# Kernel tuning notes

Measured on AMD Instinct MI355X. Metric: run time of the kernel, lower is better.

## Reference

```python
import jax, jax.numpy as jnp
import numpy as np

NUM_HEADS = 16
HEAD_DIM = 32  # out_ch 512 / 16 heads

def _c(x):
    # last axis holds (real, imag) -> complex64
    return jax.lax.complex(x[..., 0], x[..., 1])

def setup_inputs() -> dict:
    key = jax.random.key(0)
    ks = jax.random.split(key, 9)
    B, S, C = 1, 2048, 512
    mk = lambda k, shp: jax.random.normal(k, shp, dtype=jnp.float32)
    return {
        "Q": mk(ks[0], (B, S, C, 2)),
        "V": mk(ks[1], (B, S, C, 2)),
        "K": mk(ks[2], (B, S, C, 2)),
        "Wq": mk(ks[3], (C, C, 2)) * (1.0 / np.sqrt(C)),
        "bq": mk(ks[4], (C, 2)) * 0.02,
        "Wk": mk(ks[5], (C, C, 2)) * (1.0 / np.sqrt(C)),
        "bk": mk(ks[6], (C, 2)) * 0.02,
        "Wv": mk(ks[7], (C, C, 2)) * (1.0 / np.sqrt(C)),
        "bv": mk(ks[8], (C, 2)) * 0.02,
    }

def _split_heads(x):
    B, S, D = x.shape
    return x.reshape(B, S, NUM_HEADS, HEAD_DIM).transpose(0, 2, 1, 3)  # [B,H,S,d]

def reference(Q, V, K, Wq, bq, Wk, bk, Wv, bv):
    Qc, Kc, Vc = _c(Q), _c(K), _c(V)
    # torch Linear: y = x @ W^T + b, W is [out, in]
    proj = lambda x, W, b: jnp.einsum('bsi,oi->bso', x, _c(W)) + _c(b)
    q = _split_heads(proj(Qc, Wq, bq))  # [B,H,S,d] complex64
    k = _split_heads(proj(Kc, Wk, bk))
    v = _split_heads(proj(Vc, Wv, bv))
    scores = jnp.einsum('bhqd,bhkd->bhqk', q, jnp.conj(k)) / np.sqrt(HEAD_DIM).astype(np.float32)
    weights = jax.nn.softmax(jnp.abs(scores), axis=-1)  # real [B,H,S,S]
    out = jnp.einsum('bhqk,bhkd->bhqd', weights.astype(v.dtype), v)  # complex
    B, H, S, d = out.shape
    out = out.transpose(0, 2, 1, 3).reshape(B, S, H * d)  # [B,S,out_ch]
    return jnp.stack([out.real, out.imag], axis=-1)  # [B,S,out_ch,2] float32
```

## Files before the change

kernel.cpp:

```cpp
#include <hip/hip_runtime.h>
#include <hip/hip_bf16.h>
#include <math.h>

#define S_LEN 2048
#define C_DIM 512
#define NH 16
#define HD 32
#define PLANE_U (NH * S_LEN * HD)
#define WPL 262144

typedef __attribute__((ext_vector_type(8)))  short bf16x8;
typedef __attribute__((ext_vector_type(4)))  float f32x4;
typedef __attribute__((ext_vector_type(16))) float f32x16;
typedef __attribute__((ext_vector_type(4)))  unsigned int u32x4;

#if __has_builtin(__builtin_amdgcn_exp2f)
#define EXP2(x) __builtin_amdgcn_exp2f(x)
#else
#define EXP2(x) exp2f(x)
#endif

__device__ __forceinline__ unsigned int pk_bf16(float a, float b) {
    float2 f; f.x = a; f.y = b;
    __hip_bfloat162 t = __float22bfloat162_rn(f);
    return *reinterpret_cast<unsigned int*>(&t);
}

__global__ __launch_bounds__(256)
void wcvt(const float* __restrict__ Wq, const float* __restrict__ Wk,
          const float* __restrict__ Wv, unsigned short* __restrict__ ws)
{
    const int tid = blockIdx.x*256 + threadIdx.x;
    const int z   = tid >> 15;
    const int rem = tid & 32767;
    const int row = rem >> 6;
    const int kc  = (rem & 63) * 8;
    const float2* w2 = (const float2*)(z == 0 ? Wq : (z == 1 ? Wk : Wv));
    const float4* s4 = (const float4*)(w2 + (size_t)row*C_DIM + kc);
    float4 f0 = s4[0], f1 = s4[1], f2v = s4[2], f3 = s4[3];
    float re[8] = {f0.x,f0.z,f1.x,f1.z,f2v.x,f2v.z,f3.x,f3.z};
    float im[8] = {f0.y,f0.w,f1.y,f1.w,f2v.y,f2v.w,f3.y,f3.w};
    u32x4 rh, ih;
    #pragma unroll
    for (int p2 = 0; p2 < 4; ++p2) {
        rh[p2] = pk_bf16(re[2*p2], re[2*p2+1]);
        ih[p2] = pk_bf16(im[2*p2], im[2*p2+1]);
    }
    unsigned short* wf = ws + 6*(size_t)PLANE_U;
    const size_t off = (size_t)row*C_DIM + kc;
    *(u32x4*)&wf[(size_t)(z*2+0)*WPL + off] = rh;
    *(u32x4*)&wf[(size_t)(z*2+1)*WPL + off] = ih;
}

#define PROW2 72

__global__ __launch_bounds__(256)
void proj_mfma(const float* __restrict__ Q, const float* __restrict__ V,
               const float* __restrict__ K,
               const float* __restrict__ bq, const float* __restrict__ bk,
               const float* __restrict__ bv,
               unsigned short* __restrict__ ws)
{
    const int z = blockIdx.z;
    const float *X, *b;
    if (z == 0)      { X = Q; b = bq; }
    else if (z == 1) { X = K; b = bk; }
    else             { X = V; b = bv; }

    const int s0 = blockIdx.x * 64;
    const int o0 = blockIdx.y * 64;

    const float2* Bsrc = (const float2*)X;
    const unsigned short* wf = ws + 6*(size_t)PLANE_U;
    const size_t pb = (size_t)z*2*WPL;

    __shared__ __align__(16) unsigned short LBrh[64*PROW2], LBih[64*PROW2];

    const int t    = threadIdx.x;
    const int wave = t >> 6;
    const int lr   = t & 15;
    const int g    = (t & 63) >> 4;
    const int srow = t >> 2;
    const int skc  = (t & 3) * 16;

    const f32x4 zf = {0.f,0.f,0.f,0.f};
    f32x4 accR[4], accI[4];
    #pragma unroll
    for (int i = 0; i < 4; ++i) { accR[i] = zf; accI[i] = zf; }

    const size_t arow = (size_t)(o0 + wave*16 + lr) * C_DIM;

    for (int k0 = 0; k0 < C_DIM; k0 += 64) {
        const size_t ak = arow + k0 + g*8;
        bf16x8 aRH0 = *(const bf16x8*)&wf[pb + ak];
        bf16x8 aRH1 = *(const bf16x8*)&wf[pb + ak + 32];
        bf16x8 aIH0 = *(const bf16x8*)&wf[pb + WPL + ak];
        bf16x8 aIH1 = *(const bf16x8*)&wf[pb + WPL + ak + 32];
        bf16x8 aIHn0, aIHn1;
        #pragma unroll
        for (int j = 0; j < 4; ++j) {
            ((unsigned int*)&aIHn0)[j] = ((const unsigned int*)&aIH0)[j] ^ 0x80008000u;
            ((unsigned int*)&aIHn1)[j] = ((const unsigned int*)&aIH1)[j] ^ 0x80008000u;
        }

        __syncthreads();
        {
            const float4* s4 = (const float4*)(Bsrc + (size_t)(s0 + srow)*C_DIM + k0 + skc);
            u32x4 rhA, ihA, rhB, ihB;
            #pragma unroll
            for (int p2 = 0; p2 < 4; ++p2) {
                float4 fa = s4[2*p2], fb = s4[2*p2+1];
                unsigned int rw = pk_bf16(fa.x, fa.z);
                unsigned int r2 = pk_bf16(fb.x, fb.z);
                unsigned int iw = pk_bf16(fa.y, fa.w);
                unsigned int i2 = pk_bf16(fb.y, fb.w);
                if (p2 < 2) { rhA[2*p2] = rw; rhA[2*p2+1] = r2; ihA[2*p2] = iw; ihA[2*p2+1] = i2; }
                else        { rhB[2*(p2-2)] = rw; rhB[2*(p2-2)+1] = r2; ihB[2*(p2-2)] = iw; ihB[2*(p2-2)+1] = i2; }
            }
            int wb = srow*PROW2 + skc;
            *(u32x4*)&LBrh[wb]     = rhA;
            *(u32x4*)&LBrh[wb + 8] = rhB;
            *(u32x4*)&LBih[wb]     = ihA;
            *(u32x4*)&LBih[wb + 8] = ihB;
        }
        __syncthreads();

        #pragma unroll
        for (int tile = 0; tile < 4; ++tile) {
            const int bb = (tile*16 + lr)*PROW2 + g*8;
            bf16x8 bRH0 = *(const bf16x8*)&LBrh[bb];
            bf16x8 bIH0 = *(const bf16x8*)&LBih[bb];
            bf16x8 bRH1 = *(const bf16x8*)&LBrh[bb + 32];
            bf16x8 bIH1 = *(const bf16x8*)&LBih[bb + 32];
            accR[tile] = __builtin_amdgcn_mfma_f32_16x16x32_bf16(aRH0,  bRH0, accR[tile], 0,0,0);
            accR[tile] = __builtin_amdgcn_mfma_f32_16x16x32_bf16(aIHn0, bIH0, accR[tile], 0,0,0);
            accI[tile] = __builtin_amdgcn_mfma_f32_16x16x32_bf16(aRH0,  bIH0, accI[tile], 0,0,0);
            accI[tile] = __builtin_amdgcn_mfma_f32_16x16x32_bf16(aIH0,  bRH0, accI[tile], 0,0,0);
            accR[tile] = __builtin_amdgcn_mfma_f32_16x16x32_bf16(aRH1,  bRH1, accR[tile], 0,0,0);
            accR[tile] = __builtin_amdgcn_mfma_f32_16x16x32_bf16(aIHn1, bIH1, accR[tile], 0,0,0);
            accI[tile] = __builtin_amdgcn_mfma_f32_16x16x32_bf16(aRH1,  bIH1, accI[tile], 0,0,0);
            accI[tile] = __builtin_amdgcn_mfma_f32_16x16x32_bf16(aIH1,  bRH1, accI[tile], 0,0,0);
        }
    }

    const float2* b2 = (const float2*)b;
    const int obase = o0 + wave*16 + g*4;
    const int hh = obase >> 5, d0 = obase & 31;
    float bR[4], bI[4];
    #pragma unroll
    for (int r = 0; r < 4; ++r) { float2 bb = b2[obase + r]; bR[r] = bb.x; bI[r] = bb.y; }

    if (z == 0) {
        const float osc = 0.2550348677f;
        unsigned short* pr = ws;
        unsigned short* pi = pr + PLANE_U;
        #pragma unroll
        for (int tile = 0; tile < 4; ++tile) {
            int s = s0 + tile*16 + lr;
            size_t idx = ((size_t)hh*S_LEN + s)*HD + d0;
            uint2 pkR, pkI;
            pkR.x = pk_bf16((accR[tile][0]+bR[0])*osc, (accR[tile][1]+bR[1])*osc);
            pkR.y = pk_bf16((accR[tile][2]+bR[2])*osc, (accR[tile][3]+bR[3])*osc);
            pkI.x = pk_bf16((accI[tile][0]+bI[0])*osc, (accI[tile][1]+bI[1])*osc);
            pkI.y = pk_bf16((accI[tile][2]+bI[2])*osc, (accI[tile][3]+bI[3])*osc);
            *(uint2*)&pr[idx] = pkR;
            *(uint2*)&pi[idx] = pkI;
        }
    } else if (z == 1) {
        unsigned short* kf = ws + 2*(size_t)PLANE_U;
        const int frag_re = (d0 >= 16) ? 1 : 0;
        const int bsel    = (d0 & 15) >> 3;
        const int e       = d0 & 7;
        #pragma unroll
        for (int tile = 0; tile < 4; ++tile) {
            int s = s0 + tile*16 + lr;
            int c = s >> 5;
            int i = s & 31;
            int r = (i & ~12) | ((i & 4) << 1) | ((i & 8) >> 1);
            int lane = bsel*32 + r;
            size_t base = ((size_t)(hh*64 + c)*4)*512 + lane*8 + e;
            uint2 pkR, pkI;
            pkR.x = pk_bf16(accR[tile][0]+bR[0], accR[tile][1]+bR[1]);
            pkR.y = pk_bf16(accR[tile][2]+bR[2], accR[tile][3]+bR[3]);
            pkI.x = pk_bf16(accI[tile][0]+bI[0], accI[tile][1]+bI[1]);
            pkI.y = pk_bf16(accI[tile][2]+bI[2], accI[tile][3]+bI[3]);
            *(uint2*)&kf[base + (size_t)frag_re*512]     = pkR;
            *(uint2*)&kf[base + (size_t)(2+frag_re)*512] = pkI;
        }
    } else {
        unsigned short* vf = ws + 4*(size_t)PLANE_U;
        const int bsel = lr >> 3;
        const int e    = lr & 7;
        #pragma unroll
        for (int tile = 0; tile < 4; ++tile) {
            int s = s0 + tile*16 + lr;
            const int c       = s >> 5;
            const int frag_re = (s & 31) >= 16 ? 1 : 0;
            const size_t cb   = ((size_t)(hh*64 + c)*4)*512;
            #pragma unroll
            for (int r = 0; r < 4; ++r) {
                int lane = bsel*32 + d0 + r;
                size_t base = cb + (size_t)lane*8 + e;
                vf[base + (size_t)frag_re*512]     =
                    (unsigned short)pk_bf16(accR[tile][r]+bR[r], 0.f);
                vf[base + (size_t)(2+frag_re)*512] =
                    (unsigned short)pk_bf16(accI[tile][r]+bI[r], 0.f);
            }
        }
    }
}

#define RROW 33

__global__ __launch_bounds__(256, 4)
void attn_mfma(const unsigned short* __restrict__ ws, float* __restrict__ out)
{
    const int bid   = blockIdx.x;
    const int h     = bid & (NH - 1);
    const int qblk  = bid >> 4;
    const int wave  = threadIdx.x >> 6;
    const int l     = threadIdx.x & 63;
    const int q     = l & 31;
    const int b     = l >> 5;

    const unsigned short* qr = ws + 0*(size_t)PLANE_U + (size_t)h*S_LEN*HD;
    const unsigned short* qi = ws + 1*(size_t)PLANE_U + (size_t)h*S_LEN*HD;
    const unsigned short* kf = ws + 2*(size_t)PLANE_U + ((size_t)h << 17);
    const unsigned short* vf = ws + 4*(size_t)PLANE_U + ((size_t)h << 17);

    const int q0 = qblk * 32;

    bf16x8 bQr_lo = *(const bf16x8*)&qr[(size_t)(q0 + q)*HD + b*8];
    bf16x8 bQr_hi = *(const bf16x8*)&qr[(size_t)(q0 + q)*HD + 16 + b*8];
    bf16x8 bQi_lo = *(const bf16x8*)&qi[(size_t)(q0 + q)*HD + b*8];
    bf16x8 bQi_hi = *(const bf16x8*)&qi[(size_t)(q0 + q)*HD + 16 + b*8];

    __shared__ __align__(16) float2 red[2*32*RROW];

    f32x16 accR, accI;
    #pragma unroll
    for (int r = 0; r < 16; ++r) { accR[r] = 0.f; accI[r] = 0.f; }
    float lsum = 0.f;

    const f32x16 z16 = {0,0,0,0,0,0,0,0,0,0,0,0,0,0,0,0};
    const int kbeg = wave * 512;
    for (int k0 = kbeg; k0 < kbeg + 512; k0 += 32) {
        const size_t fb = (size_t)(k0 >> 5) * 2048 + l*8;

        bf16x8 aVr_lo = *(const bf16x8*)&vf[fb];
        bf16x8 aVr_hi = *(const bf16x8*)&vf[fb + 512];
        bf16x8 aVi_lo = *(const bf16x8*)&vf[fb + 1024];
        bf16x8 aVi_hi = *(const bf16x8*)&vf[fb + 1536];

        bf16x8 aKr_lo = *(const bf16x8*)&kf[fb];
        bf16x8 aKr_hi = *(const bf16x8*)&kf[fb + 512];
        bf16x8 aKi_lo = *(const bf16x8*)&kf[fb + 1024];
        bf16x8 aKi_hi = *(const bf16x8*)&kf[fb + 1536];
        bf16x8 aKin_lo, aKin_hi;
        #pragma unroll
        for (int j = 0; j < 4; ++j) {
            ((unsigned int*)&aKin_lo)[j] = ((const unsigned int*)&aKi_lo)[j] ^ 0x80008000u;
            ((unsigned int*)&aKin_hi)[j] = ((const unsigned int*)&aKi_hi)[j] ^ 0x80008000u;
        }
        f32x16 sR = __builtin_amdgcn_mfma_f32_32x32x16_bf16(aKr_lo,  bQr_lo, z16, 0, 0, 0);
        f32x16 sI = __builtin_amdgcn_mfma_f32_32x32x16_bf16(aKin_lo, bQr_lo, z16, 0, 0, 0);
        sR = __builtin_amdgcn_mfma_f32_32x32x16_bf16(aKr_hi,  bQr_hi, sR, 0, 0, 0);
        sI = __builtin_amdgcn_mfma_f32_32x32x16_bf16(aKin_hi, bQr_hi, sI, 0, 0, 0);
        sR = __builtin_amdgcn_mfma_f32_32x32x16_bf16(aKi_lo,  bQi_lo, sR, 0, 0, 0);
        sI = __builtin_amdgcn_mfma_f32_32x32x16_bf16(aKr_lo,  bQi_lo, sI, 0, 0, 0);
        sR = __builtin_amdgcn_mfma_f32_32x32x16_bf16(aKi_hi,  bQi_hi, sR, 0, 0, 0);
        sI = __builtin_amdgcn_mfma_f32_32x32x16_bf16(aKr_hi,  bQi_hi, sI, 0, 0, 0);

        bf16x8 bP1, bP2;
        unsigned int* p1 = (unsigned int*)&bP1;
        unsigned int* p2 = (unsigned int*)&bP2;
        #pragma unroll
        for (int r2 = 0; r2 < 8; ++r2) {
            int r = 2*r2;
            float v0 = EXP2(__builtin_amdgcn_sqrtf(fmaf(sR[r],   sR[r],   sI[r]*sI[r])));
            float v1 = EXP2(__builtin_amdgcn_sqrtf(fmaf(sR[r+1], sR[r+1], sI[r+1]*sI[r+1])));
            lsum += v0 + v1;
            if (r2 < 4) p1[r2]     = pk_bf16(v0, v1);
            else        p2[r2 - 4] = pk_bf16(v0, v1);
        }
        accR = __builtin_amdgcn_mfma_f32_32x32x16_bf16(aVr_lo, bP1, accR, 0, 0, 0);
        accI = __builtin_amdgcn_mfma_f32_32x32x16_bf16(aVi_lo, bP1, accI, 0, 0, 0);
        accR = __builtin_amdgcn_mfma_f32_32x32x16_bf16(aVr_hi, bP2, accR, 0, 0, 0);
        accI = __builtin_amdgcn_mfma_f32_32x32x16_bf16(aVi_hi, bP2, accI, 0, 0, 0);
    }

    lsum += __shfl_xor(lsum, 32);

    const int rrow = ((wave & 1) * 32 + q) * RROW;
    __syncthreads();
    if (wave < 2) {
        #pragma unroll
        for (int r = 0; r < 16; ++r) {
            int d = (r & 3) + 8*(r >> 2) + 4*b;
            red[rrow + d] = make_float2(accR[r], accI[r]);
        }
        if (b == 0) red[rrow + 32].x = lsum;
    }
    __syncthreads();
    if (wave >= 2) {
        #pragma unroll
        for (int r = 0; r < 16; ++r) {
            int d = (r & 3) + 8*(r >> 2) + 4*b;
            float2 v = red[rrow + d];
            v.x += accR[r]; v.y += accI[r];
            red[rrow + d] = v;
        }
        if (b == 0) red[rrow + 32].x += lsum;
    }
    __syncthreads();

    {
        const int i  = threadIdx.x;
        const int oq = i >> 3;
        const int d0 = (i & 7) * 4;
        float sl = red[oq*RROW + 32].x + red[(32 + oq)*RROW + 32].x;
        float inv = 1.0f / sl;
        float2* o2 = (float2*)out;
        #pragma unroll
        for (int dd = 0; dd < 4; ++dd) {
            int d = d0 + dd;
            float2 v0 = red[oq*RROW + d];
            float2 v1 = red[(32 + oq)*RROW + d];
            o2[(size_t)(q0 + oq)*C_DIM + h*HD + d] =
                make_float2((v0.x + v1.x)*inv, (v0.y + v1.y)*inv);
        }
    }
}

extern "C" void kernel_launch(void* const* d_in, const int* in_sizes, int n_in,
                              void* d_out, int out_size, void* d_ws, size_t ws_size,
                              hipStream_t stream)
{
    const float* Q  = (const float*)d_in[0];
    const float* V  = (const float*)d_in[1];
    const float* K  = (const float*)d_in[2];
    const float* Wq = (const float*)d_in[3];
    const float* bq = (const float*)d_in[4];
    const float* Wk = (const float*)d_in[5];
    const float* bk = (const float*)d_in[6];
    const float* Wv = (const float*)d_in[7];
    const float* bv = (const float*)d_in[8];
    unsigned short* ws = (unsigned short*)d_ws;
    float* out = (float*)d_out;

    wcvt<<<384, 256, 0, stream>>>(Wq, Wk, Wv, ws);
    proj_mfma<<<dim3(S_LEN/64, C_DIM/64, 3), 256, 0, stream>>>(Q, V, K, bq, bk, bv, ws);
    attn_mfma<<<dim3(64*NH), 256, 0, stream>>>(ws, out);
}
```

Baseline: 85.28 us.

## Split projection K-loop across two 256-thread groups with LDS reduction

The projection kernel now launches 512 threads per block. Each half processes half of the 512-wide reduction dimension into its own LDS staging buffers, then the partial accumulators are combined through shared memory before one half writes the bias-added outputs. This halves the serial K-loop length per block to raise latency hiding and wave count, at the cost of an extra LDS round-trip reduction, more barriers, and higher per-block shared memory.

```diff
diff --git a/kernel.cpp b/kernel.cpp
--- a/kernel.cpp
+++ b/kernel.cpp
@@ -54,7 +54,7 @@
 
 #define PROW2 72
 
-__global__ __launch_bounds__(256)
+__global__ __launch_bounds__(512, 6)
 void proj_mfma(const float* __restrict__ Q, const float* __restrict__ V,
                const float* __restrict__ K,
                const float* __restrict__ bq, const float* __restrict__ bk,
@@ -74,14 +74,16 @@
     const unsigned short* wf = ws + 6*(size_t)PLANE_U;
     const size_t pb = (size_t)z*2*WPL;
 
-    __shared__ __align__(16) unsigned short LBrh[64*PROW2], LBih[64*PROW2];
+    __shared__ __align__(16) unsigned short LB[2][2][64*PROW2];
 
     const int t    = threadIdx.x;
-    const int wave = t >> 6;
+    const int grp  = t >> 8;
+    const int tg   = t & 255;
+    const int wave = tg >> 6;
     const int lr   = t & 15;
     const int g    = (t & 63) >> 4;
-    const int srow = t >> 2;
-    const int skc  = (t & 3) * 16;
+    const int srow = tg >> 2;
+    const int skc  = (tg & 3) * 16;
 
     const f32x4 zf = {0.f,0.f,0.f,0.f};
     f32x4 accR[4], accI[4];
@@ -89,8 +91,10 @@
     for (int i = 0; i < 4; ++i) { accR[i] = zf; accI[i] = zf; }
 
     const size_t arow = (size_t)(o0 + wave*16 + lr) * C_DIM;
-
-    for (int k0 = 0; k0 < C_DIM; k0 += 64) {
+    const int kbase = grp * 256;
+
+    for (int it = 0; it < 4; ++it) {
+        const int k0 = kbase + it*64;
         const size_t ak = arow + k0 + g*8;
         bf16x8 aRH0 = *(const bf16x8*)&wf[pb + ak];
         bf16x8 aRH1 = *(const bf16x8*)&wf[pb + ak + 32];
@@ -118,20 +122,20 @@
                 else        { rhB[2*(p2-2)] = rw; rhB[2*(p2-2)+1] = r2; ihB[2*(p2-2)] = iw; ihB[2*(p2-2)+1] = i2; }
             }
             int wb = srow*PROW2 + skc;
-            *(u32x4*)&LBrh[wb]     = rhA;
-            *(u32x4*)&LBrh[wb + 8] = rhB;
-            *(u32x4*)&LBih[wb]     = ihA;
-            *(u32x4*)&LBih[wb + 8] = ihB;
+            *(u32x4*)&LB[grp][0][wb]     = rhA;
+            *(u32x4*)&LB[grp][0][wb + 8] = rhB;
+            *(u32x4*)&LB[grp][1][wb]     = ihA;
+            *(u32x4*)&LB[grp][1][wb + 8] = ihB;
         }
         __syncthreads();
 
         #pragma unroll
         for (int tile = 0; tile < 4; ++tile) {
             const int bb = (tile*16 + lr)*PROW2 + g*8;
-            bf16x8 bRH0 = *(const bf16x8*)&LBrh[bb];
-            bf16x8 bIH0 = *(const bf16x8*)&LBih[bb];
-            bf16x8 bRH1 = *(const bf16x8*)&LBrh[bb + 32];
-            bf16x8 bIH1 = *(const bf16x8*)&LBih[bb + 32];
+            bf16x8 bRH0 = *(const bf16x8*)&LB[grp][0][bb];
+            bf16x8 bIH0 = *(const bf16x8*)&LB[grp][1][bb];
+            bf16x8 bRH1 = *(const bf16x8*)&LB[grp][0][bb + 32];
+            bf16x8 bIH1 = *(const bf16x8*)&LB[grp][1][bb + 32];
             accR[tile] = __builtin_amdgcn_mfma_f32_16x16x32_bf16(aRH0,  bRH0, accR[tile], 0,0,0);
             accR[tile] = __builtin_amdgcn_mfma_f32_16x16x32_bf16(aIHn0, bIH0, accR[tile], 0,0,0);
             accI[tile] = __builtin_amdgcn_mfma_f32_16x16x32_bf16(aRH0,  bIH0, accI[tile], 0,0,0);
@@ -143,68 +147,92 @@
         }
     }
 
-    const float2* b2 = (const float2*)b;
-    const int obase = o0 + wave*16 + g*4;
-    const int hh = obase >> 5, d0 = obase & 31;
-    float bR[4], bI[4];
-    #pragma unroll
-    for (int r = 0; r < 4; ++r) { float2 bb = b2[obase + r]; bR[r] = bb.x; bI[r] = bb.y; }
-
-    if (z == 0) {
-        const float osc = 0.2550348677f;
-        unsigned short* pr = ws;
-        unsigned short* pi = pr + PLANE_U;
-        #pragma unroll
-        for (int tile = 0; tile < 4; ++tile) {
-            int s = s0 + tile*16 + lr;
-            size_t idx = ((size_t)hh*S_LEN + s)*HD + d0;
-            uint2 pkR, pkI;
-            pkR.x = pk_bf16((accR[tile][0]+bR[0])*osc, (accR[tile][1]+bR[1])*osc);
-            pkR.y = pk_bf16((accR[tile][2]+bR[2])*osc, (accR[tile][3]+bR[3])*osc);
-            pkI.x = pk_bf16((accI[tile][0]+bI[0])*osc, (accI[tile][1]+bI[1])*osc);
-            pkI.y = pk_bf16((accI[tile][2]+bI[2])*osc, (accI[tile][3]+bI[3])*osc);
-            *(uint2*)&pr[idx] = pkR;
-            *(uint2*)&pi[idx] = pkI;
-        }
-    } else if (z == 1) {
-        unsigned short* kf = ws + 2*(size_t)PLANE_U;
-        const int frag_re = (d0 >= 16) ? 1 : 0;
-        const int bsel    = (d0 & 15) >> 3;
-        const int e       = d0 & 7;
-        #pragma unroll
-        for (int tile = 0; tile < 4; ++tile) {
-            int s = s0 + tile*16 + lr;
-            int c = s >> 5;
-            int i = s & 31;
-            int r = (i & ~12) | ((i & 4) << 1) | ((i & 8) >> 1);
-            int lane = bsel*32 + r;
-            size_t base = ((size_t)(hh*64 + c)*4)*512 + lane*8 + e;
-            uint2 pkR, pkI;
-            pkR.x = pk_bf16(accR[tile][0]+bR[0], accR[tile][1]+bR[1]);
-            pkR.y = pk_bf16(accR[tile][2]+bR[2], accR[tile][3]+bR[3]);
-            pkI.x = pk_bf16(accI[tile][0]+bI[0], accI[tile][1]+bI[1]);
-            pkI.y = pk_bf16(accI[tile][2]+bI[2], accI[tile][3]+bI[3]);
-            *(uint2*)&kf[base + (size_t)frag_re*512]     = pkR;
-            *(uint2*)&kf[base + (size_t)(2+frag_re)*512] = pkI;
-        }
-    } else {
-        unsigned short* vf = ws + 4*(size_t)PLANE_U;
-        const int bsel = lr >> 3;
-        const int e    = lr & 7;
-        #pragma unroll
-        for (int tile = 0; tile < 4; ++tile) {
-            int s = s0 + tile*16 + lr;
-            const int c       = s >> 5;
-            const int frag_re = (s & 31) >= 16 ? 1 : 0;
-            const size_t cb   = ((size_t)(hh*64 + c)*4)*512;
+    __syncthreads();
+    float* cmb = (float*)&LB[0][0][0];
+    if (grp == 0) {
+        const int rbase = tg * 33;
+        #pragma unroll
+        for (int tile = 0; tile < 4; ++tile)
             #pragma unroll
             for (int r = 0; r < 4; ++r) {
-                int lane = bsel*32 + d0 + r;
-                size_t base = cb + (size_t)lane*8 + e;
-                vf[base + (size_t)frag_re*512]     =
-                    (unsigned short)pk_bf16(accR[tile][r]+bR[r], 0.f);
-                vf[base + (size_t)(2+frag_re)*512] =
-                    (unsigned short)pk_bf16(accI[tile][r]+bI[r], 0.f);
+                cmb[rbase + tile*8 + r]     = accR[tile][r];
+                cmb[rbase + tile*8 + 4 + r] = accI[tile][r];
+            }
+    }
+    __syncthreads();
+    if (grp == 1) {
+        const int rbase = tg * 33;
+        #pragma unroll
+        for (int tile = 0; tile < 4; ++tile)
+            #pragma unroll
+            for (int r = 0; r < 4; ++r) {
+                accR[tile][r] += cmb[rbase + tile*8 + r];
+                accI[tile][r] += cmb[rbase + tile*8 + 4 + r];
+            }
+
+        const float2* b2 = (const float2*)b;
+        const int obase = o0 + wave*16 + g*4;
+        const int hh = obase >> 5, d0 = obase & 31;
+        float bR[4], bI[4];
+        #pragma unroll
+        for (int r = 0; r < 4; ++r) { float2 bb = b2[obase + r]; bR[r] = bb.x; bI[r] = bb.y; }
+
+        if (z == 0) {
+            const float osc = 0.2550348677f;
+            unsigned short* pr = ws;
+            unsigned short* pi = pr + PLANE_U;
+            #pragma unroll
+            for (int tile = 0; tile < 4; ++tile) {
+                int s = s0 + tile*16 + lr;
+                size_t idx = ((size_t)hh*S_LEN + s)*HD + d0;
+                uint2 pkR, pkI;
+                pkR.x = pk_bf16((accR[tile][0]+bR[0])*osc, (accR[tile][1]+bR[1])*osc);
+                pkR.y = pk_bf16((accR[tile][2]+bR[2])*osc, (accR[tile][3]+bR[3])*osc);
+                pkI.x = pk_bf16((accI[tile][0]+bI[0])*osc, (accI[tile][1]+bI[1])*osc);
+                pkI.y = pk_bf16((accI[tile][2]+bI[2])*osc, (accI[tile][3]+bI[3])*osc);
+                *(uint2*)&pr[idx] = pkR;
+                *(uint2*)&pi[idx] = pkI;
+            }
+        } else if (z == 1) {
+            unsigned short* kf = ws + 2*(size_t)PLANE_U;
+            const int frag_re = (d0 >= 16) ? 1 : 0;
+            const int bsel    = (d0 & 15) >> 3;
+            const int e       = d0 & 7;
+            #pragma unroll
+            for (int tile = 0; tile < 4; ++tile) {
+                int s = s0 + tile*16 + lr;
+                int c = s >> 5;
+                int i = s & 31;
+                int r = (i & ~12) | ((i & 4) << 1) | ((i & 8) >> 1);
+                int lane = bsel*32 + r;
+                size_t base = ((size_t)(hh*64 + c)*4)*512 + lane*8 + e;
+                uint2 pkR, pkI;
+                pkR.x = pk_bf16(accR[tile][0]+bR[0], accR[tile][1]+bR[1]);
+                pkR.y = pk_bf16(accR[tile][2]+bR[2], accR[tile][3]+bR[3]);
+                pkI.x = pk_bf16(accI[tile][0]+bI[0], accI[tile][1]+bI[1]);
+                pkI.y = pk_bf16(accI[tile][2]+bI[2], accI[tile][3]+bI[3]);
+                *(uint2*)&kf[base + (size_t)frag_re*512]     = pkR;
+                *(uint2*)&kf[base + (size_t)(2+frag_re)*512] = pkI;
+            }
+        } else {
+            unsigned short* vf = ws + 4*(size_t)PLANE_U;
+            const int bsel = lr >> 3;
+            const int e    = lr & 7;
+            #pragma unroll
+            for (int tile = 0; tile < 4; ++tile) {
+                int s = s0 + tile*16 + lr;
+                const int c       = s >> 5;
+                const int frag_re = (s & 31) >= 16 ? 1 : 0;
+                const size_t cb   = ((size_t)(hh*64 + c)*4)*512;
+                #pragma unroll
+                for (int r = 0; r < 4; ++r) {
+                    int lane = bsel*32 + d0 + r;
+                    size_t base = cb + (size_t)lane*8 + e;
+                    vf[base + (size_t)frag_re*512]     =
+                        (unsigned short)pk_bf16(accR[tile][r]+bR[r], 0.f);
+                    vf[base + (size_t)(2+frag_re)*512] =
+                        (unsigned short)pk_bf16(accI[tile][r]+bI[r], 0.f);
+                }
             }
         }
     }
@@ -349,6 +377,6 @@
     float* out = (float*)d_out;
 
     wcvt<<<384, 256, 0, stream>>>(Wq, Wk, Wv, ws);
-    proj_mfma<<<dim3(S_LEN/64, C_DIM/64, 3), 256, 0, stream>>>(Q, V, K, bq, bk, bv, ws);
+    proj_mfma<<<dim3(S_LEN/64, C_DIM/64, 3), 512, 0, stream>>>(Q, V, K, bq, bk, bv, ws);
     attn_mfma<<<dim3(64*NH), 256, 0, stream>>>(ws, out);
 }
```

Result: slower. 98.24 us (+15.2%).

## Pre-convert inputs to MFMA-fragment bf16 layout and drop LDS staging in projection

Applied to the files above, without the earlier changes.

Adds an xcvt kernel that converts the Q/K/V fp32 complex inputs to bf16 real/imag planes stored directly in MFMA fragment order, and changes wcvt to emit the weights in the same fragment layout. The projection kernel then loads A and B operands straight from global memory with coalesced 16-byte loads, with no LDS staging and no __syncthreads. The sequence tile shrinks from 64 to 32, which doubles the grid. The cost is an extra launch plus a write and read of the bf16 copy of the inputs. The projection also re-reads the X fragments once per output-column block with no LDS reuse.

```diff
diff --git a/kernel.cpp b/kernel.cpp
--- a/kernel.cpp
+++ b/kernel.cpp
@@ -7,7 +7,9 @@
 #define NH 16
 #define HD 32
 #define PLANE_U (NH * S_LEN * HD)
-#define WPL 262144
+#define XF_OFF  (6*(size_t)PLANE_U)
+#define WF_OFF  (12*(size_t)PLANE_U)
+#define WPLF 262144
 
 typedef __attribute__((ext_vector_type(8)))  short bf16x8;
 typedef __attribute__((ext_vector_type(4)))  float f32x4;
@@ -27,120 +29,109 @@
 }
 
 __global__ __launch_bounds__(256)
+void xcvt(const float* __restrict__ Q, const float* __restrict__ K,
+          const float* __restrict__ V, unsigned short* __restrict__ ws)
+{
+    const int tid  = blockIdx.x*256 + threadIdx.x;
+    const int z    = tid >> 17;
+    const int rem  = tid & 131071;
+    const int kidx = rem >> 11;
+    const int s    = rem & 2047;
+    const int k    = kidx * 8;
+    const float2* x2 = (const float2*)(z == 0 ? Q : (z == 1 ? K : V));
+    const float4* s4 = (const float4*)(x2 + (size_t)s*C_DIM + k);
+    float4 f0 = s4[0], f1 = s4[1], f2v = s4[2], f3 = s4[3];
+    u32x4 rh, ih;
+    rh[0] = pk_bf16(f0.x, f0.z); rh[1] = pk_bf16(f1.x, f1.z);
+    rh[2] = pk_bf16(f2v.x, f2v.z); rh[3] = pk_bf16(f3.x, f3.z);
+    ih[0] = pk_bf16(f0.y, f0.w); ih[1] = pk_bf16(f1.y, f1.w);
+    ih[2] = pk_bf16(f2v.y, f2v.w); ih[3] = pk_bf16(f3.y, f3.w);
+    const int sb = s >> 4, lr = s & 15, g = kidx & 3, kc = kidx >> 2;
+    const size_t off = ((size_t)(sb*16 + kc)*64 + g*16 + lr)*8;
+    unsigned short* base = ws + XF_OFF + (size_t)z*2*PLANE_U;
+    *(u32x4*)&base[off]           = rh;
+    *(u32x4*)&base[PLANE_U + off] = ih;
+}
+
+__global__ __launch_bounds__(256)
 void wcvt(const float* __restrict__ Wq, const float* __restrict__ Wk,
           const float* __restrict__ Wv, unsigned short* __restrict__ ws)
 {
-    const int tid = blockIdx.x*256 + threadIdx.x;
-    const int z   = tid >> 15;
-    const int rem = tid & 32767;
-    const int row = rem >> 6;
-    const int kc  = (rem & 63) * 8;
+    const int tid  = blockIdx.x*256 + threadIdx.x;
+    const int z    = tid >> 15;
+    const int rem  = tid & 32767;
+    const int kidx = rem >> 9;
+    const int o    = rem & 511;
+    const int k    = kidx * 8;
     const float2* w2 = (const float2*)(z == 0 ? Wq : (z == 1 ? Wk : Wv));
-    const float4* s4 = (const float4*)(w2 + (size_t)row*C_DIM + kc);
+    const float4* s4 = (const float4*)(w2 + (size_t)o*C_DIM + k);
     float4 f0 = s4[0], f1 = s4[1], f2v = s4[2], f3 = s4[3];
-    float re[8] = {f0.x,f0.z,f1.x,f1.z,f2v.x,f2v.z,f3.x,f3.z};
-    float im[8] = {f0.y,f0.w,f1.y,f1.w,f2v.y,f2v.w,f3.y,f3.w};
     u32x4 rh, ih;
-    #pragma unroll
-    for (int p2 = 0; p2 < 4; ++p2) {
-        rh[p2] = pk_bf16(re[2*p2], re[2*p2+1]);
-        ih[p2] = pk_bf16(im[2*p2], im[2*p2+1]);
-    }
-    unsigned short* wf = ws + 6*(size_t)PLANE_U;
-    const size_t off = (size_t)row*C_DIM + kc;
-    *(u32x4*)&wf[(size_t)(z*2+0)*WPL + off] = rh;
-    *(u32x4*)&wf[(size_t)(z*2+1)*WPL + off] = ih;
-}
-
-#define PROW2 72
+    rh[0] = pk_bf16(f0.x, f0.z); rh[1] = pk_bf16(f1.x, f1.z);
+    rh[2] = pk_bf16(f2v.x, f2v.z); rh[3] = pk_bf16(f3.x, f3.z);
+    ih[0] = pk_bf16(f0.y, f0.w); ih[1] = pk_bf16(f1.y, f1.w);
+    ih[2] = pk_bf16(f2v.y, f2v.w); ih[3] = pk_bf16(f3.y, f3.w);
+    const int ob = o >> 4, lr = o & 15, g = kidx & 3, kc = kidx >> 2;
+    const size_t off = ((size_t)(ob*16 + kc)*64 + g*16 + lr)*8;
+    unsigned short* base = ws + WF_OFF + (size_t)z*2*WPLF;
+    *(u32x4*)&base[off]       = rh;
+    *(u32x4*)&base[WPLF + off] = ih;
+}
 
 __global__ __launch_bounds__(256)
-void proj_mfma(const float* __restrict__ Q, const float* __restrict__ V,
-               const float* __restrict__ K,
-               const float* __restrict__ bq, const float* __restrict__ bk,
+void proj_mfma(const float* __restrict__ bq, const float* __restrict__ bk,
                const float* __restrict__ bv,
                unsigned short* __restrict__ ws)
 {
     const int z = blockIdx.z;
-    const float *X, *b;
-    if (z == 0)      { X = Q; b = bq; }
-    else if (z == 1) { X = K; b = bk; }
-    else             { X = V; b = bv; }
-
-    const int s0 = blockIdx.x * 64;
+    const float* b = (z == 0) ? bq : (z == 1 ? bk : bv);
+
+    const int s0 = blockIdx.x * 32;
     const int o0 = blockIdx.y * 64;
 
-    const float2* Bsrc = (const float2*)X;
-    const unsigned short* wf = ws + 6*(size_t)PLANE_U;
-    const size_t pb = (size_t)z*2*WPL;
-
-    __shared__ __align__(16) unsigned short LBrh[64*PROW2], LBih[64*PROW2];
+    const unsigned short* xfR = ws + XF_OFF + (size_t)z*2*PLANE_U;
+    const unsigned short* xfI = xfR + PLANE_U;
+    const unsigned short* wfR = ws + WF_OFF + (size_t)z*2*WPLF;
+    const unsigned short* wfI = wfR + WPLF;
 
     const int t    = threadIdx.x;
     const int wave = t >> 6;
+    const int lane = t & 63;
     const int lr   = t & 15;
     const int g    = (t & 63) >> 4;
-    const int srow = t >> 2;
-    const int skc  = (t & 3) * 16;
+
+    const int ob = (o0 >> 4) + wave;
+    const int sb = s0 >> 4;
 
     const f32x4 zf = {0.f,0.f,0.f,0.f};
-    f32x4 accR[4], accI[4];
+    f32x4 accR[2], accI[2];
     #pragma unroll
-    for (int i = 0; i < 4; ++i) { accR[i] = zf; accI[i] = zf; }
-
-    const size_t arow = (size_t)(o0 + wave*16 + lr) * C_DIM;
-
-    for (int k0 = 0; k0 < C_DIM; k0 += 64) {
-        const size_t ak = arow + k0 + g*8;
-        bf16x8 aRH0 = *(const bf16x8*)&wf[pb + ak];
-        bf16x8 aRH1 = *(const bf16x8*)&wf[pb + ak + 32];
-        bf16x8 aIH0 = *(const bf16x8*)&wf[pb + WPL + ak];
-        bf16x8 aIH1 = *(const bf16x8*)&wf[pb + WPL + ak + 32];
-        bf16x8 aIHn0, aIHn1;
-        #pragma unroll
-        for (int j = 0; j < 4; ++j) {
-            ((unsigned int*)&aIHn0)[j] = ((const unsigned int*)&aIH0)[j] ^ 0x80008000u;
-            ((unsigned int*)&aIHn1)[j] = ((const unsigned int*)&aIH1)[j] ^ 0x80008000u;
-        }
-
-        __syncthreads();
-        {
-            const float4* s4 = (const float4*)(Bsrc + (size_t)(s0 + srow)*C_DIM + k0 + skc);
-            u32x4 rhA, ihA, rhB, ihB;
-            #pragma unroll
-            for (int p2 = 0; p2 < 4; ++p2) {
-                float4 fa = s4[2*p2], fb = s4[2*p2+1];
-                unsigned int rw = pk_bf16(fa.x, fa.z);
-                unsigned int r2 = pk_bf16(fb.x, fb.z);
-                unsigned int iw = pk_bf16(fa.y, fa.w);
-                unsigned int i2 = pk_bf16(fb.y, fb.w);
-                if (p2 < 2) { rhA[2*p2] = rw; rhA[2*p2+1] = r2; ihA[2*p2] = iw; ihA[2*p2+1] = i2; }
-                else        { rhB[2*(p2-2)] = rw; rhB[2*(p2-2)+1] = r2; ihB[2*(p2-2)] = iw; ihB[2*(p2-2)+1] = i2; }
-            }
-            int wb = srow*PROW2 + skc;
-            *(u32x4*)&LBrh[wb]     = rhA;
-            *(u32x4*)&LBrh[wb + 8] = rhB;
-            *(u32x4*)&LBih[wb]     = ihA;
-            *(u32x4*)&LBih[wb + 8] = ihB;
-        }
-        __syncthreads();
-
-        #pragma unroll
-        for (int tile = 0; tile < 4; ++tile) {
-            const int bb = (tile*16 + lr)*PROW2 + g*8;
-            bf16x8 bRH0 = *(const bf16x8*)&LBrh[bb];
-            bf16x8 bIH0 = *(const bf16x8*)&LBih[bb];
-            bf16x8 bRH1 = *(const bf16x8*)&LBrh[bb + 32];
-            bf16x8 bIH1 = *(const bf16x8*)&LBih[bb + 32];
-            accR[tile] = __builtin_amdgcn_mfma_f32_16x16x32_bf16(aRH0,  bRH0, accR[tile], 0,0,0);
-            accR[tile] = __builtin_amdgcn_mfma_f32_16x16x32_bf16(aIHn0, bIH0, accR[tile], 0,0,0);
-            accI[tile] = __builtin_amdgcn_mfma_f32_16x16x32_bf16(aRH0,  bIH0, accI[tile], 0,0,0);
-            accI[tile] = __builtin_amdgcn_mfma_f32_16x16x32_bf16(aIH0,  bRH0, accI[tile], 0,0,0);
-            accR[tile] = __builtin_amdgcn_mfma_f32_16x16x32_bf16(aRH1,  bRH1, accR[tile], 0,0,0);
-            accR[tile] = __builtin_amdgcn_mfma_f32_16x16x32_bf16(aIHn1, bIH1, accR[tile], 0,0,0);
-            accI[tile] = __builtin_amdgcn_mfma_f32_16x16x32_bf16(aRH1,  bIH1, accI[tile], 0,0,0);
-            accI[tile] = __builtin_amdgcn_mfma_f32_16x16x32_bf16(aIH1,  bRH1, accI[tile], 0,0,0);
-        }
+    for (int i = 0; i < 2; ++i) { accR[i] = zf; accI[i] = zf; }
+
+    for (int kc = 0; kc < 16; ++kc) {
+        const size_t aoff = ((size_t)(ob*16 + kc)*64 + lane)*8;
+        bf16x8 aRH = *(const bf16x8*)&wfR[aoff];
+        bf16x8 aIH = *(const bf16x8*)&wfI[aoff];
+        bf16x8 aIHn;
+        #pragma unroll
+        for (int j = 0; j < 4; ++j)
+            ((unsigned int*)&aIHn)[j] = ((const unsigned int*)&aIH)[j] ^ 0x80008000u;
+
+        const size_t b0 = ((size_t)(sb*16 + kc)*64 + lane)*8;
+        const size_t b1 = ((size_t)((sb+1)*16 + kc)*64 + lane)*8;
+        bf16x8 bRH0 = *(const bf16x8*)&xfR[b0];
+        bf16x8 bIH0 = *(const bf16x8*)&xfI[b0];
+        bf16x8 bRH1 = *(const bf16x8*)&xfR[b1];
+        bf16x8 bIH1 = *(const bf16x8*)&xfI[b1];
+
+        accR[0] = __builtin_amdgcn_mfma_f32_16x16x32_bf16(aRH,  bRH0, accR[0], 0,0,0);
+        accR[0] = __builtin_amdgcn_mfma_f32_16x16x32_bf16(aIHn, bIH0, accR[0], 0,0,0);
+        accI[0] = __builtin_amdgcn_mfma_f32_16x16x32_bf16(aRH,  bIH0, accI[0], 0,0,0);
+        accI[0] = __builtin_amdgcn_mfma_f32_16x16x32_bf16(aIH,  bRH0, accI[0], 0,0,0);
+        accR[1] = __builtin_amdgcn_mfma_f32_16x16x32_bf16(aRH,  bRH1, accR[1], 0,0,0);
+        accR[1] = __builtin_amdgcn_mfma_f32_16x16x32_bf16(aIHn, bIH1, accR[1], 0,0,0);
+        accI[1] = __builtin_amdgcn_mfma_f32_16x16x32_bf16(aRH,  bIH1, accI[1], 0,0,0);
+        accI[1] = __builtin_amdgcn_mfma_f32_16x16x32_bf16(aIH,  bRH1, accI[1], 0,0,0);
     }
 
     const float2* b2 = (const float2*)b;
@@ -155,7 +146,7 @@
         unsigned short* pr = ws;
         unsigned short* pi = pr + PLANE_U;
         #pragma unroll
-        for (int tile = 0; tile < 4; ++tile) {
+        for (int tile = 0; tile < 2; ++tile) {
             int s = s0 + tile*16 + lr;
             size_t idx = ((size_t)hh*S_LEN + s)*HD + d0;
             uint2 pkR, pkI;
@@ -172,13 +163,13 @@
         const int bsel    = (d0 & 15) >> 3;
         const int e       = d0 & 7;
         #pragma unroll
-        for (int tile = 0; tile < 4; ++tile) {
+        for (int tile = 0; tile < 2; ++tile) {
             int s = s0 + tile*16 + lr;
             int c = s >> 5;
             int i = s & 31;
             int r = (i & ~12) | ((i & 4) << 1) | ((i & 8) >> 1);
-            int lane = bsel*32 + r;
-            size_t base = ((size_t)(hh*64 + c)*4)*512 + lane*8 + e;
+            int lane2 = bsel*32 + r;
+            size_t base = ((size_t)(hh*64 + c)*4)*512 + lane2*8 + e;
             uint2 pkR, pkI;
             pkR.x = pk_bf16(accR[tile][0]+bR[0], accR[tile][1]+bR[1]);
             pkR.y = pk_bf16(accR[tile][2]+bR[2], accR[tile][3]+bR[3]);
@@ -192,15 +183,15 @@
         const int bsel = lr >> 3;
         const int e    = lr & 7;
         #pragma unroll
-        for (int tile = 0; tile < 4; ++tile) {
+        for (int tile = 0; tile < 2; ++tile) {
             int s = s0 + tile*16 + lr;
             const int c       = s >> 5;
             const int frag_re = (s & 31) >= 16 ? 1 : 0;
             const size_t cb   = ((size_t)(hh*64 + c)*4)*512;
             #pragma unroll
             for (int r = 0; r < 4; ++r) {
-                int lane = bsel*32 + d0 + r;
-                size_t base = cb + (size_t)lane*8 + e;
+                int lane2 = bsel*32 + d0 + r;
+                size_t base = cb + (size_t)lane2*8 + e;
                 vf[base + (size_t)frag_re*512]     =
                     (unsigned short)pk_bf16(accR[tile][r]+bR[r], 0.f);
                 vf[base + (size_t)(2+frag_re)*512] =
@@ -348,7 +339,8 @@
     unsigned short* ws = (unsigned short*)d_ws;
     float* out = (float*)d_out;
 
+    xcvt<<<1536, 256, 0, stream>>>(Q, K, V, ws);
     wcvt<<<384, 256, 0, stream>>>(Wq, Wk, Wv, ws);
-    proj_mfma<<<dim3(S_LEN/64, C_DIM/64, 3), 256, 0, stream>>>(Q, V, K, bq, bk, bv, ws);
+    proj_mfma<<<dim3(S_LEN/32, C_DIM/64, 3), 256, 0, stream>>>(bq, bk, bv, ws);
     attn_mfma<<<dim3(64*NH), 256, 0, stream>>>(ws, out);
 }
```

Result: faster. 78.21 us (-8.3%).
